# Kernel optimization log

Measured on AMD Instinct MI355X. Metric: run time of the kernel, lower is better.

## Reference

```python
import jax, jax.numpy as jnp
import numpy as np

D_MODEL = 1024
NUM_HEADS = 16
THETA = 10000.0
B, T = 2, 2048


def _rope(x, pos, theta_base):
    # x: (b, h, t, d_h); interleaved pairs (x0,x1),(x2,x3),... per the
    # rearrange '... (c d) -> ... c d' with d=2 in the original module.
    d = x.shape[-1]
    half = d // 2
    inv_freq = 1.0 / (theta_base ** (2.0 * jnp.arange(half, dtype=jnp.float32) / d))
    ang = pos.astype(jnp.float32)[:, None] * inv_freq[None, :]  # (t, half)
    sin = jnp.sin(ang)[None, None]  # (1,1,t,half)
    cos = jnp.cos(ang)[None, None]
    x1 = x[..., 0::2]
    x2 = x[..., 1::2]
    r1 = x1 * cos - x2 * sin
    r2 = x1 * sin + x2 * cos
    return jnp.stack([r1, r2], axis=-1).reshape(x.shape)


def setup_inputs() -> dict:
    key = jax.random.key(0)
    k0, k1, k2, k3, k4 = jax.random.split(key, 5)
    sigma = (2.0 / (D_MODEL + D_MODEL)) ** 0.5
    return {
        "in_features": jax.random.normal(k0, (B, T, D_MODEL), dtype=jnp.float32),
        "Wq": jax.random.normal(k1, (D_MODEL, D_MODEL), dtype=jnp.float32) * sigma,
        "Wk": jax.random.normal(k2, (D_MODEL, D_MODEL), dtype=jnp.float32) * sigma,
        "Wv": jax.random.normal(k3, (D_MODEL, D_MODEL), dtype=jnp.float32) * sigma,
        "Wo": jax.random.normal(k4, (D_MODEL, D_MODEL), dtype=jnp.float32) * sigma,
        "token_positions": jnp.arange(T, dtype=jnp.int32),
    }


def reference(in_features, Wq, Wk, Wv, Wo, token_positions):
    b, t, d_model = in_features.shape
    h = NUM_HEADS
    d_h = d_model // h
    # Fused-style QKV projections (x @ W.T, weights stored (in, out))
    q = in_features @ Wq.T
    k = in_features @ Wk.T
    v = in_features @ Wv.T
    # (b, t, h*d_h) -> (b, h, t, d_h)
    q = q.reshape(b, t, h, d_h).transpose(0, 2, 1, 3)
    k = k.reshape(b, t, h, d_h).transpose(0, 2, 1, 3)
    v = v.reshape(b, t, h, d_h).transpose(0, 2, 1, 3)
    q = _rope(q, token_positions, THETA)
    k = _rope(k, token_positions, THETA)
    scale = 1.0 / jnp.sqrt(jnp.asarray(d_h, dtype=q.dtype))
    scores = jnp.einsum('bhqd,bhkd->bhqk', q, k) * scale
    causal = jnp.tril(jnp.ones((t, t), dtype=bool))
    scores = jnp.where(causal[None, None], scores, -jnp.inf)
    attn = jax.nn.softmax(scores, axis=-1)
    out = jnp.einsum('bhqk,bhkd->bhqd', attn, v)
    out = out.transpose(0, 2, 1, 3).reshape(b, t, h * d_h)
    return out @ Wo.T
```

## Files before the change

### kernel.cpp

```cpp
#include <hip/hip_runtime.h>

#define D_MODEL 1024
#define NUM_HEADS 16
#define DH 64
#define B_SZ 2
#define T_SZ 2048
#define M_ROWS (B_SZ * T_SZ)

typedef __bf16 bf16;
typedef __bf16 bf16x4 __attribute__((ext_vector_type(4)));
typedef __bf16 bf16x8 __attribute__((ext_vector_type(8)));
typedef float f32x4 __attribute__((ext_vector_type(4)));

__device__ __forceinline__ void async_copy16(const bf16* g, bf16* l) {
  __builtin_amdgcn_global_load_lds(
      (const __attribute__((address_space(1))) void*)g,
      (__attribute__((address_space(3))) void*)l, 16, 0, 0);
}

#define NX (M_ROWS * D_MODEL / 4)
#define NW (D_MODEL * D_MODEL / 4)

__global__ __launch_bounds__(256) void cast_all(
    const float* __restrict__ X, const float* __restrict__ Wq,
    const float* __restrict__ Wk, const float* __restrict__ Wv,
    const float* __restrict__ Wo,
    bf16* __restrict__ Xb, bf16* __restrict__ Wqb, bf16* __restrict__ Wkb,
    bf16* __restrict__ Wvb, bf16* __restrict__ Wob) {
  int i = blockIdx.x * 256 + threadIdx.x;
  const float* s; bf16* d; int off;
  if (i < NX) {
    s = X; d = Xb; off = i;
  } else {
    int j = i - NX;
    int w = j >> 18;
    off = j & (NW - 1);
    if (w == 0)      { s = Wq; d = Wqb; }
    else if (w == 1) { s = Wk; d = Wkb; }
    else if (w == 2) { s = Wv; d = Wvb; }
    else             { s = Wo; d = Wob; }
  }
  float4 v = ((const float4*)s)[off];
  bf16x4 o;
  o[0] = (bf16)v.x; o[1] = (bf16)v.y; o[2] = (bf16)v.z; o[3] = (bf16)v.w;
  ((bf16x4*)d)[off] = o;
}

__global__ __launch_bounds__(256) void qkv_gemm(
    const bf16* __restrict__ Xb,
    const bf16* __restrict__ Wqb, const bf16* __restrict__ Wkb,
    const bf16* __restrict__ Wvb,
    bf16* __restrict__ Q, bf16* __restrict__ K, bf16* __restrict__ V) {
  __shared__ bf16 As[128 * 32];
  __shared__ bf16 Bs[128 * 32];

  int tid = threadIdx.x;
  int wave = tid >> 6, lane = tid & 63;
  int wm = wave >> 1, wn = wave & 1;
  int l15 = lane & 15, quad = lane >> 4;

  int row0 = blockIdx.x * 128;
  int col0 = blockIdx.y * 128;
  int sel = col0 >> 10;
  int nb = col0 & 1023;
  const bf16* W; bf16* Out;
  if (sel == 0)      { W = Wqb; Out = Q; }
  else if (sel == 1) { W = Wkb; Out = K; }
  else               { W = Wvb; Out = V; }

  int srow = tid >> 2;
  int schunk = tid & 3;
  const bf16* Ag = Xb + (size_t)(row0 + srow) * D_MODEL + schunk * 8;
  const bf16* Bg = W + (size_t)(nb + srow) * D_MODEL + schunk * 8;
  bf16* Al0 = &As[srow * 32 + schunk * 8];
  bf16* Al1 = &As[(srow + 64) * 32 + schunk * 8];
  bf16* Bl0 = &Bs[srow * 32 + schunk * 8];
  bf16* Bl1 = &Bs[(srow + 64) * 32 + schunk * 8];

  f32x4 acc[4][4];
#pragma unroll
  for (int i = 0; i < 4; ++i)
#pragma unroll
    for (int j = 0; j < 4; ++j) acc[i][j] = (f32x4){0.f, 0.f, 0.f, 0.f};

  for (int k0 = 0; k0 < D_MODEL; k0 += 32) {
    async_copy16(Ag + k0, Al0);
    async_copy16(Ag + k0 + (size_t)64 * D_MODEL, Al1);
    async_copy16(Bg + k0, Bl0);
    async_copy16(Bg + k0 + (size_t)64 * D_MODEL, Bl1);
    __syncthreads();

    bf16x8 af[4], bfr[4];
#pragma unroll
    for (int i = 0; i < 4; ++i)
      af[i] = *(const bf16x8*)&As[(wm * 64 + i * 16 + l15) * 32 + quad * 8];
#pragma unroll
    for (int j = 0; j < 4; ++j)
      bfr[j] = *(const bf16x8*)&Bs[(wn * 64 + j * 16 + l15) * 32 + quad * 8];
#pragma unroll
    for (int i = 0; i < 4; ++i)
#pragma unroll
      for (int j = 0; j < 4; ++j)
        acc[i][j] = __builtin_amdgcn_mfma_f32_16x16x32_bf16(af[i], bfr[j],
                                                            acc[i][j], 0, 0, 0);
    __syncthreads();
  }

#pragma unroll
  for (int i = 0; i < 4; ++i) {
    int row = row0 + wm * 64 + i * 16 + quad * 4;
#pragma unroll
    for (int j = 0; j < 4; ++j) {
      int col = nb + wn * 64 + j * 16 + l15;
#pragma unroll
      for (int r = 0; r < 4; ++r)
        Out[(size_t)(row + r) * D_MODEL + col] = (bf16)acc[i][j][r];
    }
  }
}

__global__ __launch_bounds__(256) void rope_kernel(
    bf16* __restrict__ Q, bf16* __restrict__ K, const int* __restrict__ pos) {
  int idx = blockIdx.x * 256 + threadIdx.x;
  int i = idx & 31;
  int h = (idx >> 5) & 15;
  int row = idx >> 9;
  int t = row & (T_SZ - 1);
  float p = (float)pos[t];
  float freq = expf(-(float)i * 0.28782313662425f);
  float ang = p * freq;
  float s, c;
  sincosf(ang, &s, &c);
  size_t base = (size_t)row * D_MODEL + h * DH + 2 * i;
  float q1 = (float)Q[base], q2 = (float)Q[base + 1];
  Q[base]     = (bf16)(q1 * c - q2 * s);
  Q[base + 1] = (bf16)(q1 * s + q2 * c);
  float k1 = (float)K[base], k2 = (float)K[base + 1];
  K[base]     = (bf16)(k1 * c - k2 * s);
  K[base + 1] = (bf16)(k1 * s + k2 * c);
}

__global__ __launch_bounds__(256) void v_transpose(
    const bf16* __restrict__ V, bf16* __restrict__ VT) {
  __shared__ bf16 tile[64][72];
  int bh = blockIdx.x;
  int tt = blockIdx.y;
  int b = bh >> 4, h = bh & 15;
  int tid = threadIdx.x;
  int rr = tid >> 3;
  int cc = (tid & 7) * 8;
#pragma unroll
  for (int p = 0; p < 2; ++p) {
    int t = rr + p * 32;
    bf16x8 v = *(const bf16x8*)&V[((size_t)b * T_SZ + tt * 64 + t) * D_MODEL +
                                  h * DH + cc];
    *(bf16x8*)&tile[t][cc] = v;
  }
  __syncthreads();
#pragma unroll
  for (int p = 0; p < 2; ++p) {
    int d = rr + p * 32;
    bf16x8 o;
#pragma unroll
    for (int j = 0; j < 8; ++j) o[j] = tile[cc + j][d];
    *(bf16x8*)&VT[((size_t)bh * DH + d) * T_SZ + tt * 64 + cc] = o;
  }
}

#define PST 72

__global__ __launch_bounds__(256) void attn_kernel(
    const bf16* __restrict__ Q, const bf16* __restrict__ K,
    const bf16* __restrict__ VT, bf16* __restrict__ AO) {
  __shared__ bf16 Kt0[64 * 32], Kt1[64 * 32];
  __shared__ bf16 Vt0[64 * 32], Vt1[64 * 32];
  __shared__ bf16 Pbuf[4][16 * PST];

  int bh = blockIdx.x;
  int qi = 31 - (int)blockIdx.y;
  int bb = bh >> 4, h = bh & 15;
  int tid = threadIdx.x;
  int wave = tid >> 6, lane = tid & 63;
  int l15 = lane & 15, quad = lane >> 4;

  int q0 = qi * 64 + wave * 16;
  size_t grow = (size_t)bb * T_SZ + q0;

  const bf16* Qp = Q + (grow + l15) * D_MODEL + h * DH + quad * 8;
  bf16x8 bq0 = *(const bf16x8*)(Qp);
  bf16x8 bq1 = *(const bf16x8*)(Qp + 32);

  f32x4 o[4];
#pragma unroll
  for (int nt = 0; nt < 4; ++nt) o[nt] = (f32x4){0.f, 0.f, 0.f, 0.f};
  float l_i = 0.f;

  int srow = tid >> 2;
  int sch = tid & 3;
  const bf16* Kg = K + ((size_t)bb * T_SZ + srow) * D_MODEL + h * DH + sch * 8;
  const bf16* Vg = VT + ((size_t)bh * DH + srow) * T_SZ + sch * 8;
  bf16* Kl0 = &Kt0[srow * 32 + sch * 8];
  bf16* Kl1 = &Kt1[srow * 32 + sch * 8];
  bf16* Vl0 = &Vt0[srow * 32 + sch * 8];
  bf16* Vl1 = &Vt1[srow * 32 + sch * 8];

  bf16* Pw = Pbuf[wave];
  int nchunks = qi + 1;
  int rel = wave * 16 + l15;

  for (int t = 0; t < nchunks; ++t) {
    int kv0 = t * 64;

    async_copy16(Kg + (size_t)kv0 * D_MODEL, Kl0);
    async_copy16(Kg + (size_t)kv0 * D_MODEL + 32, Kl1);
    async_copy16(Vg + kv0, Vl0);
    async_copy16(Vg + kv0 + 32, Vl1);
    __syncthreads();

    f32x4 st[4];
#pragma unroll
    for (int cs = 0; cs < 4; ++cs) {
      bf16x8 ak0 = *(const bf16x8*)&Kt0[(cs * 16 + l15) * 32 + quad * 8];
      bf16x8 ak1 = *(const bf16x8*)&Kt1[(cs * 16 + l15) * 32 + quad * 8];
      f32x4 s = (f32x4){0.f, 0.f, 0.f, 0.f};
      s = __builtin_amdgcn_mfma_f32_16x16x32_bf16(ak0, bq0, s, 0, 0, 0);
      s = __builtin_amdgcn_mfma_f32_16x16x32_bf16(ak1, bq1, s, 0, 0, 0);
      st[cs] = s;
    }

    bool last = (t == nchunks - 1);
    float ps = 0.f;
#pragma unroll
    for (int cs = 0; cs < 4; ++cs)
#pragma unroll
      for (int r = 0; r < 4; ++r) {
        float p = __expf(st[cs][r] * 0.125f);
        if (last) {
          int cl = cs * 16 + quad * 4 + r;
          p = (cl > rel) ? 0.f : p;
        }
        st[cs][r] = p;
        ps += p;
      }
    l_i += ps;

#pragma unroll
    for (int cs = 0; cs < 4; ++cs) {
      bf16x4 pk;
#pragma unroll
      for (int r = 0; r < 4; ++r) pk[r] = (bf16)st[cs][r];
      *(bf16x4*)&Pw[l15 * PST + cs * 16 + quad * 4] = pk;
    }
    __asm__ __volatile__("" ::: "memory");
    bf16x8 bp0 = *(const bf16x8*)&Pw[l15 * PST + quad * 8];
    bf16x8 bp1 = *(const bf16x8*)&Pw[l15 * PST + 32 + quad * 8];
    __asm__ __volatile__("" ::: "memory");

#pragma unroll
    for (int nt = 0; nt < 4; ++nt) {
      bf16x8 av0 = *(const bf16x8*)&Vt0[(nt * 16 + l15) * 32 + quad * 8];
      bf16x8 av1 = *(const bf16x8*)&Vt1[(nt * 16 + l15) * 32 + quad * 8];
      o[nt] = __builtin_amdgcn_mfma_f32_16x16x32_bf16(av0, bp0, o[nt], 0, 0, 0);
      o[nt] = __builtin_amdgcn_mfma_f32_16x16x32_bf16(av1, bp1, o[nt], 0, 0, 0);
    }
    __syncthreads();
  }

  l_i += __shfl_xor(l_i, 16);
  l_i += __shfl_xor(l_i, 32);
  float inv = 1.0f / l_i;
#pragma unroll
  for (int nt = 0; nt < 4; ++nt) {
    bf16x4 ov;
#pragma unroll
    for (int r = 0; r < 4; ++r) ov[r] = (bf16)(o[nt][r] * inv);
    *(bf16x4*)&AO[(grow + l15) * D_MODEL + h * DH + nt * 16 + quad * 4] = ov;
  }
}

__global__ __launch_bounds__(256) void out_gemm(
    const bf16* __restrict__ AO, const bf16* __restrict__ Wob,
    float* __restrict__ out) {
  __shared__ bf16 As[128 * 32];
  __shared__ bf16 Bs[128 * 32];

  int tid = threadIdx.x;
  int wave = tid >> 6, lane = tid & 63;
  int wm = wave >> 1, wn = wave & 1;
  int l15 = lane & 15, quad = lane >> 4;

  int row0 = blockIdx.x * 128;
  int nb = blockIdx.y * 128;

  int srow = tid >> 2;
  int schunk = tid & 3;
  const bf16* Ag = AO + (size_t)(row0 + srow) * D_MODEL + schunk * 8;
  const bf16* Bg = Wob + (size_t)(nb + srow) * D_MODEL + schunk * 8;
  bf16* Al0 = &As[srow * 32 + schunk * 8];
  bf16* Al1 = &As[(srow + 64) * 32 + schunk * 8];
  bf16* Bl0 = &Bs[srow * 32 + schunk * 8];
  bf16* Bl1 = &Bs[(srow + 64) * 32 + schunk * 8];

  f32x4 acc[4][4];
#pragma unroll
  for (int i = 0; i < 4; ++i)
#pragma unroll
    for (int j = 0; j < 4; ++j) acc[i][j] = (f32x4){0.f, 0.f, 0.f, 0.f};

  for (int k0 = 0; k0 < D_MODEL; k0 += 32) {
    async_copy16(Ag + k0, Al0);
    async_copy16(Ag + k0 + (size_t)64 * D_MODEL, Al1);
    async_copy16(Bg + k0, Bl0);
    async_copy16(Bg + k0 + (size_t)64 * D_MODEL, Bl1);
    __syncthreads();

    bf16x8 af[4], bfr[4];
#pragma unroll
    for (int i = 0; i < 4; ++i)
      af[i] = *(const bf16x8*)&As[(wm * 64 + i * 16 + l15) * 32 + quad * 8];
#pragma unroll
    for (int j = 0; j < 4; ++j)
      bfr[j] = *(const bf16x8*)&Bs[(wn * 64 + j * 16 + l15) * 32 + quad * 8];
#pragma unroll
    for (int i = 0; i < 4; ++i)
#pragma unroll
      for (int j = 0; j < 4; ++j)
        acc[i][j] = __builtin_amdgcn_mfma_f32_16x16x32_bf16(af[i], bfr[j],
                                                            acc[i][j], 0, 0, 0);
    __syncthreads();
  }

#pragma unroll
  for (int i = 0; i < 4; ++i) {
    int row = row0 + wm * 64 + i * 16 + quad * 4;
#pragma unroll
    for (int j = 0; j < 4; ++j) {
      int col = nb + wn * 64 + j * 16 + l15;
#pragma unroll
      for (int r = 0; r < 4; ++r)
        out[(size_t)(row + r) * D_MODEL + col] = acc[i][j][r];
    }
  }
}

extern "C" void kernel_launch(void* const* d_in, const int* in_sizes, int n_in,
                              void* d_out, int out_size, void* d_ws, size_t ws_size,
                              hipStream_t stream) {
  const float* X  = (const float*)d_in[0];
  const float* Wq = (const float*)d_in[1];
  const float* Wk = (const float*)d_in[2];
  const float* Wv = (const float*)d_in[3];
  const float* Wo = (const float*)d_in[4];
  const int*  pos = (const int*)d_in[5];
  float* out = (float*)d_out;

  char* w = (char*)d_ws;
  bf16* Xb  = (bf16*)w;  w += (size_t)M_ROWS * D_MODEL * 2;
  bf16* Wqb = (bf16*)w;  w += (size_t)D_MODEL * D_MODEL * 2;
  bf16* Wkb = (bf16*)w;  w += (size_t)D_MODEL * D_MODEL * 2;
  bf16* Wvb = (bf16*)w;  w += (size_t)D_MODEL * D_MODEL * 2;
  bf16* Wob = (bf16*)w;  w += (size_t)D_MODEL * D_MODEL * 2;
  bf16* Qb  = (bf16*)w;  w += (size_t)M_ROWS * D_MODEL * 2;
  bf16* Kb  = (bf16*)w;  w += (size_t)M_ROWS * D_MODEL * 2;
  bf16* Vb  = (bf16*)w;  w += (size_t)M_ROWS * D_MODEL * 2;
  bf16* AO  = (bf16*)w;  w += (size_t)M_ROWS * D_MODEL * 2;
  bf16* VT  = (bf16*)w;  w += (size_t)M_ROWS * D_MODEL * 2;

  cast_all<<<(NX + 4 * NW) / 256, 256, 0, stream>>>(X, Wq, Wk, Wv, Wo,
                                                    Xb, Wqb, Wkb, Wvb, Wob);
  qkv_gemm<<<dim3(M_ROWS / 128, 3 * D_MODEL / 128), 256, 0, stream>>>(
      Xb, Wqb, Wkb, Wvb, Qb, Kb, Vb);
  rope_kernel<<<(M_ROWS * NUM_HEADS * 32) / 256, 256, 0, stream>>>(Qb, Kb, pos);
  v_transpose<<<dim3(B_SZ * NUM_HEADS, T_SZ / 64), 256, 0, stream>>>(Vb, VT);
  attn_kernel<<<dim3(B_SZ * NUM_HEADS, T_SZ / 64), 256, 0, stream>>>(Qb, Kb, VT, AO);
  out_gemm<<<dim3(M_ROWS / 128, D_MODEL / 128), 256, 0, stream>>>(AO, Wob, out);
}
```

Before: 194.2 us.

## Fuse Q RoPE into attention, merge K RoPE with V transpose, use 128-row attention tiles

RoPE for K and the V transpose now run in one launch, and RoPE for Q is applied in registers inside the attention kernel. This removes a launch and a read/write pass over Q. The attention kernel now uses 512 threads over 128 query rows, so each K/V tile loaded into LDS is reused by eight waves instead of four, halving K/V traffic per query. In exchange, the upper waves sit idle on the final chunk and the causal load is less balanced across the smaller grid.

```diff
diff --git a/kernel.cpp b/kernel.cpp
--- a/kernel.cpp
+++ b/kernel.cpp
@@ -119,149 +119,167 @@
   }
 }
 
-__global__ __launch_bounds__(256) void rope_kernel(
-    bf16* __restrict__ Q, bf16* __restrict__ K, const int* __restrict__ pos) {
-  int idx = blockIdx.x * 256 + threadIdx.x;
-  int i = idx & 31;
-  int h = (idx >> 5) & 15;
-  int row = idx >> 9;
-  int t = row & (T_SZ - 1);
-  float p = (float)pos[t];
-  float freq = expf(-(float)i * 0.28782313662425f);
-  float ang = p * freq;
-  float s, c;
-  sincosf(ang, &s, &c);
-  size_t base = (size_t)row * D_MODEL + h * DH + 2 * i;
-  float q1 = (float)Q[base], q2 = (float)Q[base + 1];
-  Q[base]     = (bf16)(q1 * c - q2 * s);
-  Q[base + 1] = (bf16)(q1 * s + q2 * c);
-  float k1 = (float)K[base], k2 = (float)K[base + 1];
-  K[base]     = (bf16)(k1 * c - k2 * s);
-  K[base + 1] = (bf16)(k1 * s + k2 * c);
-}
-
-__global__ __launch_bounds__(256) void v_transpose(
-    const bf16* __restrict__ V, bf16* __restrict__ VT) {
-  __shared__ bf16 tile[64][72];
-  int bh = blockIdx.x;
-  int tt = blockIdx.y;
-  int b = bh >> 4, h = bh & 15;
-  int tid = threadIdx.x;
-  int rr = tid >> 3;
-  int cc = (tid & 7) * 8;
-#pragma unroll
-  for (int p = 0; p < 2; ++p) {
-    int t = rr + p * 32;
-    bf16x8 v = *(const bf16x8*)&V[((size_t)b * T_SZ + tt * 64 + t) * D_MODEL +
-                                  h * DH + cc];
-    *(bf16x8*)&tile[t][cc] = v;
-  }
-  __syncthreads();
-#pragma unroll
-  for (int p = 0; p < 2; ++p) {
-    int d = rr + p * 32;
-    bf16x8 o;
-#pragma unroll
-    for (int j = 0; j < 8; ++j) o[j] = tile[cc + j][d];
-    *(bf16x8*)&VT[((size_t)bh * DH + d) * T_SZ + tt * 64 + cc] = o;
+#define ROPEK_BLOCKS (M_ROWS * NUM_HEADS * 32 / 256)
+
+__global__ __launch_bounds__(256) void ropek_vt(
+    bf16* __restrict__ K, const bf16* __restrict__ V, bf16* __restrict__ VT,
+    const int* __restrict__ pos) {
+  int b0 = blockIdx.x;
+  if (b0 < ROPEK_BLOCKS) {
+    int idx = b0 * 256 + threadIdx.x;
+    int i = idx & 31;
+    int h = (idx >> 5) & 15;
+    int row = idx >> 9;
+    int t = row & (T_SZ - 1);
+    float p = (float)pos[t];
+    float freq = __expf(-(float)i * 0.28782313662425f);
+    float s, c;
+    sincosf(p * freq, &s, &c);
+    size_t base = (size_t)row * D_MODEL + h * DH + 2 * i;
+    float k1 = (float)K[base], k2 = (float)K[base + 1];
+    K[base]     = (bf16)(k1 * c - k2 * s);
+    K[base + 1] = (bf16)(k1 * s + k2 * c);
+  } else {
+    __shared__ bf16 tile[64][72];
+    int vb = b0 - ROPEK_BLOCKS;
+    int bh = vb >> 5;
+    int tt = vb & 31;
+    int b = bh >> 4, h = bh & 15;
+    int tid = threadIdx.x;
+    int rr = tid >> 3;
+    int cc = (tid & 7) * 8;
+#pragma unroll
+    for (int p = 0; p < 2; ++p) {
+      int t = rr + p * 32;
+      bf16x8 v = *(const bf16x8*)&V[((size_t)b * T_SZ + tt * 64 + t) * D_MODEL +
+                                    h * DH + cc];
+      *(bf16x8*)&tile[t][cc] = v;
+    }
+    __syncthreads();
+#pragma unroll
+    for (int p = 0; p < 2; ++p) {
+      int d = rr + p * 32;
+      bf16x8 o;
+#pragma unroll
+      for (int j = 0; j < 8; ++j) o[j] = tile[cc + j][d];
+      *(bf16x8*)&VT[((size_t)bh * DH + d) * T_SZ + tt * 64 + cc] = o;
+    }
   }
 }
 
 #define PST 72
 
-__global__ __launch_bounds__(256) void attn_kernel(
+__global__ __launch_bounds__(512) void attn_kernel(
     const bf16* __restrict__ Q, const bf16* __restrict__ K,
-    const bf16* __restrict__ VT, bf16* __restrict__ AO) {
+    const bf16* __restrict__ VT, const int* __restrict__ pos,
+    bf16* __restrict__ AO) {
   __shared__ bf16 Kt0[64 * 32], Kt1[64 * 32];
   __shared__ bf16 Vt0[64 * 32], Vt1[64 * 32];
-  __shared__ bf16 Pbuf[4][16 * PST];
+  __shared__ bf16 Pbuf[8][16 * PST];
 
   int bh = blockIdx.x;
-  int qi = 31 - (int)blockIdx.y;
+  int qi = 15 - (int)blockIdx.y;
   int bb = bh >> 4, h = bh & 15;
   int tid = threadIdx.x;
   int wave = tid >> 6, lane = tid & 63;
   int l15 = lane & 15, quad = lane >> 4;
 
-  int q0 = qi * 64 + wave * 16;
+  int q0 = qi * 128 + wave * 16;
   size_t grow = (size_t)bb * T_SZ + q0;
 
   const bf16* Qp = Q + (grow + l15) * D_MODEL + h * DH + quad * 8;
   bf16x8 bq0 = *(const bf16x8*)(Qp);
   bf16x8 bq1 = *(const bf16x8*)(Qp + 32);
+  {
+    float p = (float)pos[q0 + l15];
+#pragma unroll
+    for (int jj = 0; jj < 4; ++jj) {
+      int i0 = quad * 4 + jj;
+      float s, c;
+      sincosf(p * __expf(-(float)i0 * 0.28782313662425f), &s, &c);
+      float x1 = (float)bq0[2 * jj], x2 = (float)bq0[2 * jj + 1];
+      bq0[2 * jj]     = (bf16)(x1 * c - x2 * s);
+      bq0[2 * jj + 1] = (bf16)(x1 * s + x2 * c);
+      sincosf(p * __expf(-(float)(i0 + 16) * 0.28782313662425f), &s, &c);
+      float y1 = (float)bq1[2 * jj], y2 = (float)bq1[2 * jj + 1];
+      bq1[2 * jj]     = (bf16)(y1 * c - y2 * s);
+      bq1[2 * jj + 1] = (bf16)(y1 * s + y2 * c);
+    }
+  }
 
   f32x4 o[4];
 #pragma unroll
   for (int nt = 0; nt < 4; ++nt) o[nt] = (f32x4){0.f, 0.f, 0.f, 0.f};
   float l_i = 0.f;
 
-  int srow = tid >> 2;
-  int sch = tid & 3;
-  const bf16* Kg = K + ((size_t)bb * T_SZ + srow) * D_MODEL + h * DH + sch * 8;
-  const bf16* Vg = VT + ((size_t)bh * DH + srow) * T_SZ + sch * 8;
-  bf16* Kl0 = &Kt0[srow * 32 + sch * 8];
-  bf16* Kl1 = &Kt1[srow * 32 + sch * 8];
-  bf16* Vl0 = &Vt0[srow * 32 + sch * 8];
-  bf16* Vl1 = &Vt1[srow * 32 + sch * 8];
+  bool isK = (tid < 256);
+  int stid = isK ? tid : tid - 256;
+  int srow = stid >> 2, sch = stid & 3;
+  const bf16* sbase = isK
+      ? K + ((size_t)bb * T_SZ + srow) * D_MODEL + h * DH + sch * 8
+      : VT + ((size_t)bh * DH + srow) * T_SZ + sch * 8;
+  size_t sstep = isK ? (size_t)64 * D_MODEL : (size_t)64;
+  bf16* sdst0 = isK ? &Kt0[srow * 32 + sch * 8] : &Vt0[srow * 32 + sch * 8];
+  bf16* sdst1 = isK ? &Kt1[srow * 32 + sch * 8] : &Vt1[srow * 32 + sch * 8];
 
   bf16* Pw = Pbuf[wave];
-  int nchunks = qi + 1;
-  int rel = wave * 16 + l15;
+  int nchunks = 2 * qi + 2;
+  int tb = 2 * qi + (wave >> 2);
+  int bound = (wave & 3) * 16 + l15;
 
   for (int t = 0; t < nchunks; ++t) {
-    int kv0 = t * 64;
-
-    async_copy16(Kg + (size_t)kv0 * D_MODEL, Kl0);
-    async_copy16(Kg + (size_t)kv0 * D_MODEL + 32, Kl1);
-    async_copy16(Vg + kv0, Vl0);
-    async_copy16(Vg + kv0 + 32, Vl1);
-    __syncthreads();
-
-    f32x4 st[4];
-#pragma unroll
-    for (int cs = 0; cs < 4; ++cs) {
-      bf16x8 ak0 = *(const bf16x8*)&Kt0[(cs * 16 + l15) * 32 + quad * 8];
-      bf16x8 ak1 = *(const bf16x8*)&Kt1[(cs * 16 + l15) * 32 + quad * 8];
-      f32x4 s = (f32x4){0.f, 0.f, 0.f, 0.f};
-      s = __builtin_amdgcn_mfma_f32_16x16x32_bf16(ak0, bq0, s, 0, 0, 0);
-      s = __builtin_amdgcn_mfma_f32_16x16x32_bf16(ak1, bq1, s, 0, 0, 0);
-      st[cs] = s;
-    }
-
-    bool last = (t == nchunks - 1);
-    float ps = 0.f;
-#pragma unroll
-    for (int cs = 0; cs < 4; ++cs)
-#pragma unroll
-      for (int r = 0; r < 4; ++r) {
-        float p = __expf(st[cs][r] * 0.125f);
-        if (last) {
-          int cl = cs * 16 + quad * 4 + r;
-          p = (cl > rel) ? 0.f : p;
+    const bf16* s = sbase + (size_t)t * sstep;
+    async_copy16(s, sdst0);
+    async_copy16(s + 32, sdst1);
+    __syncthreads();
+
+    if (t <= tb) {
+      f32x4 st[4];
+#pragma unroll
+      for (int cs = 0; cs < 4; ++cs) {
+        bf16x8 ak0 = *(const bf16x8*)&Kt0[(cs * 16 + l15) * 32 + quad * 8];
+        bf16x8 ak1 = *(const bf16x8*)&Kt1[(cs * 16 + l15) * 32 + quad * 8];
+        f32x4 s4 = (f32x4){0.f, 0.f, 0.f, 0.f};
+        s4 = __builtin_amdgcn_mfma_f32_16x16x32_bf16(ak0, bq0, s4, 0, 0, 0);
+        s4 = __builtin_amdgcn_mfma_f32_16x16x32_bf16(ak1, bq1, s4, 0, 0, 0);
+        st[cs] = s4;
+      }
+
+      bool bm = (t == tb);
+      float ps = 0.f;
+#pragma unroll
+      for (int cs = 0; cs < 4; ++cs)
+#pragma unroll
+        for (int r = 0; r < 4; ++r) {
+          float p = __expf(st[cs][r] * 0.125f);
+          if (bm) {
+            int cl = cs * 16 + quad * 4 + r;
+            p = (cl > bound) ? 0.f : p;
+          }
+          st[cs][r] = p;
+          ps += p;
         }
-        st[cs][r] = p;
-        ps += p;
+      l_i += ps;
+
+#pragma unroll
+      for (int cs = 0; cs < 4; ++cs) {
+        bf16x4 pk;
+#pragma unroll
+        for (int r = 0; r < 4; ++r) pk[r] = (bf16)st[cs][r];
+        *(bf16x4*)&Pw[l15 * PST + cs * 16 + quad * 4] = pk;
       }
-    l_i += ps;
-
-#pragma unroll
-    for (int cs = 0; cs < 4; ++cs) {
-      bf16x4 pk;
-#pragma unroll
-      for (int r = 0; r < 4; ++r) pk[r] = (bf16)st[cs][r];
-      *(bf16x4*)&Pw[l15 * PST + cs * 16 + quad * 4] = pk;
-    }
-    __asm__ __volatile__("" ::: "memory");
-    bf16x8 bp0 = *(const bf16x8*)&Pw[l15 * PST + quad * 8];
-    bf16x8 bp1 = *(const bf16x8*)&Pw[l15 * PST + 32 + quad * 8];
-    __asm__ __volatile__("" ::: "memory");
-
-#pragma unroll
-    for (int nt = 0; nt < 4; ++nt) {
-      bf16x8 av0 = *(const bf16x8*)&Vt0[(nt * 16 + l15) * 32 + quad * 8];
-      bf16x8 av1 = *(const bf16x8*)&Vt1[(nt * 16 + l15) * 32 + quad * 8];
-      o[nt] = __builtin_amdgcn_mfma_f32_16x16x32_bf16(av0, bp0, o[nt], 0, 0, 0);
-      o[nt] = __builtin_amdgcn_mfma_f32_16x16x32_bf16(av1, bp1, o[nt], 0, 0, 0);
+      __asm__ __volatile__("" ::: "memory");
+      bf16x8 bp0 = *(const bf16x8*)&Pw[l15 * PST + quad * 8];
+      bf16x8 bp1 = *(const bf16x8*)&Pw[l15 * PST + 32 + quad * 8];
+      __asm__ __volatile__("" ::: "memory");
+
+#pragma unroll
+      for (int nt = 0; nt < 4; ++nt) {
+        bf16x8 av0 = *(const bf16x8*)&Vt0[(nt * 16 + l15) * 32 + quad * 8];
+        bf16x8 av1 = *(const bf16x8*)&Vt1[(nt * 16 + l15) * 32 + quad * 8];
+        o[nt] = __builtin_amdgcn_mfma_f32_16x16x32_bf16(av0, bp0, o[nt], 0, 0, 0);
+        o[nt] = __builtin_amdgcn_mfma_f32_16x16x32_bf16(av1, bp1, o[nt], 0, 0, 0);
+      }
     }
     __syncthreads();
   }
@@ -370,8 +388,9 @@
                                                     Xb, Wqb, Wkb, Wvb, Wob);
   qkv_gemm<<<dim3(M_ROWS / 128, 3 * D_MODEL / 128), 256, 0, stream>>>(
       Xb, Wqb, Wkb, Wvb, Qb, Kb, Vb);
-  rope_kernel<<<(M_ROWS * NUM_HEADS * 32) / 256, 256, 0, stream>>>(Qb, Kb, pos);
-  v_transpose<<<dim3(B_SZ * NUM_HEADS, T_SZ / 64), 256, 0, stream>>>(Vb, VT);
-  attn_kernel<<<dim3(B_SZ * NUM_HEADS, T_SZ / 64), 256, 0, stream>>>(Qb, Kb, VT, AO);
+  ropek_vt<<<ROPEK_BLOCKS + B_SZ * NUM_HEADS * (T_SZ / 64), 256, 0, stream>>>(
+      Kb, Vb, VT, pos);
+  attn_kernel<<<dim3(B_SZ * NUM_HEADS, T_SZ / 128), 512, 0, stream>>>(
+      Qb, Kb, VT, pos, AO);
   out_gemm<<<dim3(M_ROWS / 128, D_MODEL / 128), 256, 0, stream>>>(AO, Wob, out);
 }
```

Result: no change. 196.1 us (+1.0%).
